# Optimization experiments

Measured on AMD Instinct MI355X. Metric: run time of the kernel, lower is better.

Reference implementation:

```python
import jax, jax.numpy as jnp
import numpy as np

B, T, S, G, D, H, W, CHUNK = 2, 4096, 4096, 64, 1024, 16, 512, 256
HD = D // H


def setup_inputs() -> dict:
    key = jax.random.key(0)
    ks = jax.random.split(key, 16)
    std = 1.0 / np.sqrt(D)
    w = lambda k: jax.random.normal(k, (D, D), jnp.float32) * std
    b = lambda k: jax.random.normal(k, (D,), jnp.float32) * 0.01
    return {
        "query": jax.random.normal(ks[0], (B, T, D), jnp.float32),
        "encoder_out": jax.random.normal(ks[1], (B, S, D), jnp.float32),
        "global_tokens": jax.random.normal(ks[2], (B, G, D), jnp.float32),
        "qw": w(ks[3]), "qb": b(ks[4]),
        "kw": w(ks[5]), "kb": b(ks[6]),
        "vw": w(ks[7]), "vb": b(ks[8]),
        "gkw": w(ks[9]), "gkb": b(ks[10]),
        "gvw": w(ks[11]), "gvb": b(ks[12]),
        "ow": w(ks[13]), "ob": b(ks[14]),
        "compression_ratio": 1,
    }


def reference(query, encoder_out, global_tokens, qw, qb, kw, kb, vw, vb,
              gkw, gkb, gvw, gvb, ow, ob, compression_ratio):
    scale = jnp.float32(np.sqrt(HD))
    r = jnp.float32(compression_ratio)
    # expected raw position for each decoder step, clamped to valid src range
    expected = jnp.clip((jnp.arange(T, dtype=jnp.float32) / r).astype(jnp.int32), 0, S - 1)
    expected = jnp.broadcast_to(expected[None], (B, T))  # [B,T]

    lin = lambda x, wt, bs: x @ wt.T + bs  # torch nn.Linear: y = x W^T + b
    q = lin(query, qw, qb).reshape(B, T, H, HD).transpose(0, 2, 1, 3)            # [B,H,T,HD]
    gk = lin(global_tokens, gkw, gkb).reshape(B, G, H, HD).transpose(0, 2, 1, 3)  # [B,H,G,HD]
    gv = lin(global_tokens, gvw, gvb).reshape(B, G, H, HD).transpose(0, 2, 1, 3)
    ak = lin(encoder_out, kw, kb).reshape(B, S, H, HD).transpose(0, 2, 1, 3)      # [B,H,S,HD]
    av = lin(encoder_out, vw, vb).reshape(B, S, H, HD).transpose(0, 2, 1, 3)

    nC = T // CHUNK
    # per-(batch,chunk) window start, from the middle query's expected position
    centers = expected.reshape(B, nC, CHUNK)[:, :, CHUNK // 2]   # [B,nC]
    win_start = jnp.clip(centers - W // 2, 0, S - W)             # [B,nC]; window always full length W
    idx = win_start[:, :, None] + jnp.arange(W)[None, None, :]   # [B,nC,W]

    gather = lambda kv_b, idx_b: kv_b[:, idx_b, :]               # [H,S,HD],[nC,W] -> [H,nC,W,HD]
    wk = jax.vmap(gather)(ak, idx)                               # [B,H,nC,W,HD]
    wv = jax.vmap(gather)(av, idx)

    qc = q.reshape(B, H, nC, CHUNK, HD)
    sg = jnp.einsum('bhcqd,bhgd->bhcqg', qc, gk) / scale          # global scores  [B,H,nC,CHUNK,G]
    sl = jnp.einsum('bhcqd,bhcwd->bhcqw', qc, wk) / scale         # windowed scores [B,H,nC,CHUNK,W]
    attn = jax.nn.softmax(jnp.concatenate([sg, sl], axis=-1), axis=-1)
    out = (jnp.einsum('bhcqg,bhgd->bhcqd', attn[..., :G], gv)
           + jnp.einsum('bhcqw,bhcwd->bhcqd', attn[..., G:], wv))  # [B,H,nC,CHUNK,HD]
    out = out.reshape(B, H, T, HD).transpose(0, 2, 1, 3).reshape(B, T, D)
    return lin(out, ow, ob)
```

## Files before the change

kernel.cpp:

```cpp
#include <hip/hip_runtime.h>

typedef unsigned short u16;
typedef unsigned int u32;
typedef __attribute__((ext_vector_type(4))) float f32x4;
typedef __attribute__((ext_vector_type(16))) float f32x16;
typedef __attribute__((ext_vector_type(8))) short bf16x8;

constexpr int B_ = 2, T_ = 4096, S_ = 4096, G_ = 64, D_ = 1024, H_ = 16, W_ = 512, CHUNK_ = 256;
constexpr int NC_ = T_ / CHUNK_;
constexpr int NT_ = (G_ + W_) / 32;

__device__ __forceinline__ u16 f2bf(float x) {
  u32 u = __builtin_bit_cast(u32, x);
  return (u16)((u + 0x7FFFu + ((u >> 16) & 1u)) >> 16);
}

__global__ __launch_bounds__(256) void cvt_all_kernel(const float* __restrict__ q, const float* __restrict__ e,
                                                      const float* __restrict__ g, const float* __restrict__ w0,
                                                      const float* __restrict__ w1, const float* __restrict__ w2,
                                                      const float* __restrict__ w3, const float* __restrict__ w4,
                                                      const float* __restrict__ w5, u16* __restrict__ dst) {
  int blk = blockIdx.x;
  const float* src;
  int sblk;
  if (blk < 8192) { src = q; sblk = 0; }
  else if (blk < 16384) { src = e; sblk = 8192; }
  else if (blk < 16512) { src = g; sblk = 16384; }
  else if (blk < 17536) { src = w0; sblk = 16512; }
  else if (blk < 18560) { src = w1; sblk = 17536; }
  else if (blk < 19584) { src = w2; sblk = 18560; }
  else if (blk < 20608) { src = w3; sblk = 19584; }
  else if (blk < 21632) { src = w4; sblk = 20608; }
  else { src = w5; sblk = 21632; }
  int li = (blk - sblk) * 256 + threadIdx.x;
  size_t gi = (size_t)blk * 256 + threadIdx.x;
  float4 v = ((const float4*)src)[li];
  uint2 o;
  o.x = (u32)f2bf(v.x) | ((u32)f2bf(v.y) << 16);
  o.y = (u32)f2bf(v.z) | ((u32)f2bf(v.w) << 16);
  ((uint2*)dst)[gi] = o;
}

__global__ __launch_bounds__(512, 2) void proj_kernel(const u16* __restrict__ ex, const u16* __restrict__ qx,
                                                      const u16* __restrict__ gx, const u16* __restrict__ wgt,
                                                      const float* __restrict__ qb, const float* __restrict__ kbias,
                                                      const float* __restrict__ vbias, const float* __restrict__ gkb,
                                                      const float* __restrict__ gvb, u16* __restrict__ q_bf,
                                                      u16* __restrict__ k_bf, u16* __restrict__ gk_bf) {
  __shared__ char lds[73728];
  constexpr size_t NW = (size_t)D_ * D_;
  constexpr size_t NQs = (size_t)B_ * T_ * D_;
  constexpr size_t NGs = (size_t)B_ * G_ * D_;
  const int tid = threadIdx.x;
  const int lane = tid & 63;
  const int wid = tid >> 6;
  const int wm = wid >> 1, wn = wid & 1;
  const int l15 = lane & 15, kg = lane >> 4;

  const int bid = blockIdx.x;
  const u16 *A, *Bt;
  const float *b1, *b2;
  u16* out;
  int row0, col0, mloc;
  bool scale = false, dual = false;
  size_t dsplit = 0;
  if (bid < 512) {
    row0 = (bid & 31) * 256; col0 = (bid >> 5) * 128; mloc = 256;
    A = ex; Bt = wgt + NW; b1 = kbias; b2 = vbias; out = k_bf; dsplit = NQs; dual = true;
  } else if (bid < 768) {
    int i = bid - 512;
    row0 = (i & 31) * 256; col0 = (i >> 5) * 128; mloc = 256;
    A = qx; Bt = wgt; b1 = qb; b2 = qb; out = q_bf; scale = true;
  } else {
    int i = bid - 768;
    row0 = 0; col0 = i * 128; mloc = 128;
    A = gx; Bt = wgt + 3 * NW; b1 = gkb; b2 = gvb; out = gk_bf; dsplit = NGs; dual = true;
  }
  const float* bp = b1;
  u16* op = out;
  if (dual && col0 >= 1024) { bp = b2 - 1024; op = out + (dsplit - 1024); }

  f32x4 acc[4][4];
#pragma unroll
  for (int i = 0; i < 4; i++)
#pragma unroll
    for (int j = 0; j < 4; j++)
#pragma unroll
      for (int r = 0; r < 4; r++) acc[i][j][r] = 0.f;

  const char* Abase = (const char*)A;
  const char* Bbase = (const char*)Bt;
  const int swb = 16 * ((tid & 3) ^ ((tid >> 3) & 3));

  auto stageA = [&](int slot, int kt) {
#pragma unroll
    for (int p = 0; p < 2; p++) {
      int dst = slot * 16384 + p * 8192 + tid * 16;
      const char* g = Abase + (size_t)(row0 + p * 128 + (tid >> 2)) * 2048 + kt * 64 + swb;
      __builtin_amdgcn_global_load_lds((const __attribute__((address_space(1))) void*)g,
                                       (__attribute__((address_space(3))) void*)(lds + dst), 16, 0, 0);
    }
  };
  auto stageB = [&](int slot, int kt) {
    int dst = 49152 + slot * 8192 + tid * 16;
    const char* g = Bbase + (size_t)(col0 + (tid >> 2)) * 2048 + kt * 64 + swb;
    __builtin_amdgcn_global_load_lds((const __attribute__((address_space(1))) void*)g,
                                     (__attribute__((address_space(3))) void*)(lds + dst), 16, 0, 0);
  };

  stageA(0, 0); stageB(0, 0);
  stageA(1, 1); stageB(1, 1);
  asm volatile("s_waitcnt vmcnt(3)" ::: "memory");
  __builtin_amdgcn_s_barrier();

  int cur = 0, nx = 2;
  for (int t = 0; t < 32; ++t) {
    const char* Ab = lds + cur * 16384;
    const char* Bb = lds + 49152 + cur * 8192;
    if (t + 2 < 32) { stageA(nx, t + 2); stageB(nx, t + 2); }
    bf16x8 bq[4], af[4];
#pragma unroll
    for (int ni = 0; ni < 4; ni++) {
      int r = wn * 64 + ni * 16 + l15;
      bq[ni] = *(const bf16x8*)(Bb + ((r * 64 + kg * 16) ^ (((r >> 1) & 3) << 4)));
    }
#pragma unroll
    for (int mi = 0; mi < 4; mi++) {
      int r = wm * 64 + mi * 16 + l15;
      af[mi] = *(const bf16x8*)(Ab + ((r * 64 + kg * 16) ^ (((r >> 1) & 3) << 4)));
    }
    __builtin_amdgcn_s_setprio(1);
#pragma unroll
    for (int mi = 0; mi < 4; mi++)
#pragma unroll
      for (int ni = 0; ni < 4; ni++)
        acc[mi][ni] = __builtin_amdgcn_mfma_f32_16x16x32_bf16(bq[ni], af[mi], acc[mi][ni], 0, 0, 0);
    __builtin_amdgcn_s_setprio(0);
    if (t < 30) {
      asm volatile("s_waitcnt vmcnt(3)" ::: "memory");
    } else if (t == 30) {
      asm volatile("s_waitcnt vmcnt(0)" ::: "memory");
    }
    __builtin_amdgcn_s_barrier();
    cur = cur == 2 ? 0 : cur + 1;
    nx = nx == 2 ? 0 : nx + 1;
  }

  float4 bv4[4];
#pragma unroll
  for (int ni = 0; ni < 4; ni++) bv4[ni] = *(const float4*)&bp[col0 + wn * 64 + ni * 16 + kg * 4];
#pragma unroll
  for (int mi = 0; mi < 4; mi++) {
    int rloc = wm * 64 + mi * 16 + l15;
    if (rloc >= mloc) continue;
    size_t grow = (size_t)(row0 + rloc);
#pragma unroll
    for (int ni = 0; ni < 4; ni++) {
      int gcol = col0 + wn * 64 + ni * 16 + kg * 4;
      float v0 = acc[mi][ni][0] + bv4[ni].x;
      float v1 = acc[mi][ni][1] + bv4[ni].y;
      float v2 = acc[mi][ni][2] + bv4[ni].z;
      float v3 = acc[mi][ni][3] + bv4[ni].w;
      if (scale) {
        v0 *= 0.18033688011112042f; v1 *= 0.18033688011112042f;
        v2 *= 0.18033688011112042f; v3 *= 0.18033688011112042f;
      }
      uint2 o;
      asm("v_cvt_pk_bf16_f32 %0, %1, %2" : "=v"(o.x) : "v"(v0), "v"(v1));
      asm("v_cvt_pk_bf16_f32 %0, %1, %2" : "=v"(o.y) : "v"(v2), "v"(v3));
      *(uint2*)&op[grow * 1024 + gcol] = o;
    }
  }
}

__global__ __launch_bounds__(512, 2) void gemmO_kernel(const u16* __restrict__ A, const u16* __restrict__ Bt,
                                                       const float* __restrict__ bias, float* __restrict__ out) {
  __shared__ char lds[73728];
  const int tid = threadIdx.x;
  const int lane = tid & 63;
  const int wid = tid >> 6;
  const int wm = wid >> 1, wn = wid & 1;
  const int l15 = lane & 15, kg = lane >> 4;

  const int bid = blockIdx.x;
  const int row0 = (bid & 31) * 256;
  const int col0 = (bid >> 5) * 128;

  f32x4 acc[4][4];
#pragma unroll
  for (int i = 0; i < 4; i++)
#pragma unroll
    for (int j = 0; j < 4; j++)
#pragma unroll
      for (int r = 0; r < 4; r++) acc[i][j][r] = 0.f;

  const char* Abase = (const char*)A;
  const char* Bbase = (const char*)Bt;
  const int swb = 16 * ((tid & 3) ^ ((tid >> 3) & 3));

  auto stageA = [&](int slot, int kt) {
#pragma unroll
    for (int p = 0; p < 2; p++) {
      int dst = slot * 16384 + p * 8192 + tid * 16;
      const char* g = Abase + (size_t)(row0 + p * 128 + (tid >> 2)) * 2048 + kt * 64 + swb;
      __builtin_amdgcn_global_load_lds((const __attribute__((address_space(1))) void*)g,
                                       (__attribute__((address_space(3))) void*)(lds + dst), 16, 0, 0);
    }
  };
  auto stageB = [&](int slot, int kt) {
    int dst = 49152 + slot * 8192 + tid * 16;
    const char* g = Bbase + (size_t)(col0 + (tid >> 2)) * 2048 + kt * 64 + swb;
    __builtin_amdgcn_global_load_lds((const __attribute__((address_space(1))) void*)g,
                                     (__attribute__((address_space(3))) void*)(lds + dst), 16, 0, 0);
  };

  stageA(0, 0); stageB(0, 0);
  stageA(1, 1); stageB(1, 1);
  asm volatile("s_waitcnt vmcnt(3)" ::: "memory");
  __builtin_amdgcn_s_barrier();

  int cur = 0, nx = 2;
  for (int t = 0; t < 32; ++t) {
    const char* Ab = lds + cur * 16384;
    const char* Bb = lds + 49152 + cur * 8192;
    if (t + 2 < 32) { stageA(nx, t + 2); stageB(nx, t + 2); }
    bf16x8 bq[4], af[4];
#pragma unroll
    for (int ni = 0; ni < 4; ni++) {
      int r = wn * 64 + ni * 16 + l15;
      bq[ni] = *(const bf16x8*)(Bb + ((r * 64 + kg * 16) ^ (((r >> 1) & 3) << 4)));
    }
#pragma unroll
    for (int mi = 0; mi < 4; mi++) {
      int r = wm * 64 + mi * 16 + l15;
      af[mi] = *(const bf16x8*)(Ab + ((r * 64 + kg * 16) ^ (((r >> 1) & 3) << 4)));
    }
    __builtin_amdgcn_s_setprio(1);
#pragma unroll
    for (int mi = 0; mi < 4; mi++)
#pragma unroll
      for (int ni = 0; ni < 4; ni++)
        acc[mi][ni] = __builtin_amdgcn_mfma_f32_16x16x32_bf16(bq[ni], af[mi], acc[mi][ni], 0, 0, 0);
    __builtin_amdgcn_s_setprio(0);
    if (t < 30) {
      asm volatile("s_waitcnt vmcnt(3)" ::: "memory");
    } else if (t == 30) {
      asm volatile("s_waitcnt vmcnt(0)" ::: "memory");
    }
    __builtin_amdgcn_s_barrier();
    cur = cur == 2 ? 0 : cur + 1;
    nx = nx == 2 ? 0 : nx + 1;
  }

  float4 bv4[4];
#pragma unroll
  for (int ni = 0; ni < 4; ni++) bv4[ni] = *(const float4*)&bias[col0 + wn * 64 + ni * 16 + kg * 4];
#pragma unroll
  for (int mi = 0; mi < 4; mi++) {
    size_t grow = (size_t)(row0 + wm * 64 + mi * 16 + l15);
#pragma unroll
    for (int ni = 0; ni < 4; ni++) {
      int gcol = col0 + wn * 64 + ni * 16 + kg * 4;
      float4 fo;
      fo.x = acc[mi][ni][0] + bv4[ni].x;
      fo.y = acc[mi][ni][1] + bv4[ni].y;
      fo.z = acc[mi][ni][2] + bv4[ni].z;
      fo.w = acc[mi][ni][3] + bv4[ni].w;
      *(float4*)&out[grow * 1024 + gcol] = fo;
    }
  }
}

__global__ __launch_bounds__(512, 4) void attn_kernel(const u16* __restrict__ q_bf, const u16* __restrict__ k_bf,
                                                      const u16* __restrict__ v_bf, const u16* __restrict__ gk_bf,
                                                      const u16* __restrict__ gv_bf, u16* __restrict__ ao,
                                                      const int* __restrict__ rptr) {
  __shared__ u16 smem[16384];
  const int c = blockIdx.x, h = blockIdx.y, b = blockIdx.z;
  const int tid = threadIdx.x;
  const int lane = tid & 63, wv = tid >> 6;
  const int l31 = lane & 31, half = lane >> 5;
  const int t0 = c * CHUNK_;

  int rr = rptr[0];
  int centert = c * CHUNK_ + CHUNK_ / 2;
  int expected = (int)((float)centert / (float)rr);
  expected = min(max(expected, 0), S_ - 1);
  int ws0 = min(max(expected - W_ / 2, 0), S_ - W_);

  bf16x8 qf[4];
  {
    const u16* qrow = q_bf + ((size_t)(b * T_ + t0 + wv * 32 + l31)) * D_ + h * 64 + half * 8;
#pragma unroll
    for (int s = 0; s < 4; s++) qf[s] = *(const bf16x8*)(qrow + s * 16);
  }

  const int skey = (tid & 255) >> 3, shq = tid & 7;
  const bool isK = tid < 256;

  auto load_tile = [&](int j) -> uint4 {
    const u16* base;
    size_t row;
    if (j < 2) {
      base = isK ? gk_bf : gv_bf;
      row = (size_t)(b * G_ + j * 32 + skey);
    } else {
      base = isK ? k_bf : v_bf;
      row = (size_t)(b * S_ + ws0 + (j - 2) * 32 + skey);
    }
    return *(const uint4*)(base + row * D_ + h * 64 + shq * 8);
  };

  f32x16 oacc[2];
#pragma unroll
  for (int i = 0; i < 2; i++)
#pragma unroll
    for (int r = 0; r < 16; r++) oacc[i][r] = 0.f;
  float mrun = -1e30f, lsum = 0.f;

  uint4 stg = load_tile(0);

  for (int j = 0; j < NT_; j++) {
    const int bsel = j & 1;
    if (isK) {
      *(uint4*)((char*)smem + bsel * 4096 + ((skey * 128 + shq * 16) ^ ((skey & 7) << 4))) = stg;
    } else {
      const u16* pv = (const u16*)&stg;
      char* bp = (char*)smem + 8192 + bsel * 5248 + shq * 656 + skey * 2;
#pragma unroll
      for (int e = 0; e < 8; e++) *(u16*)(bp + e * 80) = pv[e];
    }
    if (j + 1 < NT_) stg = load_tile(j + 1);
    __syncthreads();

    const int kbase = bsel * 4096;
    const int vtb = 8192 + bsel * 5248;

    f32x16 sacc;
#pragma unroll
    for (int r = 0; r < 16; r++) sacc[r] = 0.f;
    __builtin_amdgcn_s_setprio(1);
#pragma unroll
    for (int s = 0; s < 4; s++) {
      int kbx = kbase + ((l31 * 128 + half * 16 + s * 32) ^ ((l31 & 7) << 4));
      bf16x8 kf = *(const bf16x8*)((char*)smem + kbx);
      sacc = __builtin_amdgcn_mfma_f32_32x32x16_bf16(kf, qf[s], sacc, 0, 0, 0);
    }
    __builtin_amdgcn_s_setprio(0);

    float t0m = fmaxf(fmaxf(sacc[0], sacc[1]), sacc[2]);
    float t1m = fmaxf(fmaxf(sacc[3], sacc[4]), sacc[5]);
    float t2m = fmaxf(fmaxf(sacc[6], sacc[7]), sacc[8]);
    float t3m = fmaxf(fmaxf(sacc[9], sacc[10]), sacc[11]);
    float t4m = fmaxf(fmaxf(sacc[12], sacc[13]), sacc[14]);
    float tmax = fmaxf(fmaxf(fmaxf(t0m, t1m), fmaxf(t2m, t3m)), fmaxf(t4m, sacc[15]));
    tmax = fmaxf(tmax, __shfl_xor(tmax, 32));
    if (__any(tmax > mrun + 8.f)) {
      float mnew = fmaxf(mrun, tmax);
      float fac = __builtin_amdgcn_exp2f(mrun - mnew);
      mrun = mnew;
      lsum *= fac;
#pragma unroll
      for (int i = 0; i < 2; i++)
#pragma unroll
        for (int r = 0; r < 16; r++) oacc[i][r] *= fac;
    }
    float p[16];
#pragma unroll
    for (int r = 0; r < 16; r++) p[r] = __builtin_amdgcn_exp2f(sacc[r] - mrun);
    float s0s = (p[0] + p[1]) + (p[2] + p[3]);
    float s1s = (p[4] + p[5]) + (p[6] + p[7]);
    float s2s = (p[8] + p[9]) + (p[10] + p[11]);
    float s3s = (p[12] + p[13]) + (p[14] + p[15]);
    float tsum = (s0s + s1s) + (s2s + s3s);
    tsum += __shfl_xor(tsum, 32);
    lsum += tsum;

    u32 xs[8], px[8];
#pragma unroll
    for (int i = 0; i < 8; i++)
      asm("v_cvt_pk_bf16_f32 %0, %1, %2" : "=v"(xs[i]) : "v"(p[2 * i]), "v"(p[2 * i + 1]));
#pragma unroll
    for (int i = 0; i < 8; i++) px[i] = (u32)__shfl_xor((int)xs[i], 32);
    u32 Bk[2][4];
    Bk[0][0] = half ? px[2] : xs[0];
    Bk[0][1] = half ? px[3] : xs[1];
    Bk[0][2] = half ? xs[2] : px[0];
    Bk[0][3] = half ? xs[3] : px[1];
    Bk[1][0] = half ? px[6] : xs[4];
    Bk[1][1] = half ? px[7] : xs[5];
    Bk[1][2] = half ? xs[6] : px[4];
    Bk[1][3] = half ? xs[7] : px[5];

    int vro = vtb + l31 * 80 + ((l31 >> 3) << 4) + half * 16;
    __builtin_amdgcn_s_setprio(1);
#pragma unroll
    for (int hdf = 0; hdf < 2; hdf++) {
#pragma unroll
      for (int ks = 0; ks < 2; ks++) {
        bf16x8 vf = *(const bf16x8*)((const char*)smem + vro + hdf * 2624 + ks * 32);
        uint4 u4;
        u4.x = Bk[ks][0]; u4.y = Bk[ks][1]; u4.z = Bk[ks][2]; u4.w = Bk[ks][3];
        bf16x8 pb = __builtin_bit_cast(bf16x8, u4);
        oacc[hdf] = __builtin_amdgcn_mfma_f32_32x32x16_bf16(vf, pb, oacc[hdf], 0, 0, 0);
      }
    }
    __builtin_amdgcn_s_setprio(0);
  }

  __syncthreads();
  float inv = 1.f / lsum;
#pragma unroll
  for (int hdf = 0; hdf < 2; hdf++) {
#pragma unroll
    for (int a = 0; a < 4; a++) {
      float f0 = oacc[hdf][4 * a] * inv, f1 = oacc[hdf][4 * a + 1] * inv;
      float f2 = oacc[hdf][4 * a + 2] * inv, f3 = oacc[hdf][4 * a + 3] * inv;
      uint2 o;
      asm("v_cvt_pk_bf16_f32 %0, %1, %2" : "=v"(o.x) : "v"(f0), "v"(f1));
      asm("v_cvt_pk_bf16_f32 %0, %1, %2" : "=v"(o.y) : "v"(f2), "v"(f3));
      int off = wv * 4096 + l31 * 128 + ((16 * a + 8 * half + 64 * hdf) ^ ((l31 & 7) << 4));
      *(uint2*)((char*)smem + off) = o;
    }
  }
  __syncthreads();
#pragma unroll
  for (int it = 0; it < 4; it++) {
    int byteo = (tid + it * 512) * 16;
    int row = byteo >> 7;
    int colb = byteo & 127;
    uint4 vv = *(const uint4*)((const char*)smem + row * 128 + (colb ^ ((row & 7) << 4)));
    *(uint4*)(ao + ((size_t)(b * T_ + t0 + row)) * D_ + h * 64 + (colb >> 1)) = vv;
  }
}

extern "C" void kernel_launch(void* const* d_in, const int* in_sizes, int n_in,
                              void* d_out, int out_size, void* d_ws, size_t ws_size,
                              hipStream_t stream) {
  (void)in_sizes; (void)n_in; (void)out_size; (void)ws_size;
  const float* query = (const float*)d_in[0];
  const float* enc = (const float*)d_in[1];
  const float* glob = (const float*)d_in[2];
  const float* qw = (const float*)d_in[3];
  const float* qb = (const float*)d_in[4];
  const float* kw = (const float*)d_in[5];
  const float* kb = (const float*)d_in[6];
  const float* vw = (const float*)d_in[7];
  const float* vb = (const float*)d_in[8];
  const float* gkw = (const float*)d_in[9];
  const float* gkb = (const float*)d_in[10];
  const float* gvw = (const float*)d_in[11];
  const float* gvb = (const float*)d_in[12];
  const float* ow = (const float*)d_in[13];
  const float* ob = (const float*)d_in[14];
  const int* rp = (const int*)d_in[15];

  const size_t NQ = (size_t)B_ * T_ * D_;
  const size_t NG = (size_t)B_ * G_ * D_;
  const size_t NW = (size_t)D_ * D_;

  u16* ws = (u16*)d_ws;
  u16* qx = ws;
  u16* ex = qx + NQ;
  u16* gx = ex + NQ;
  u16* wgt = gx + NG;
  u16* q_bf = wgt + 6 * NW;
  u16* k_bf = q_bf + NQ;
  u16* v_bf = k_bf + NQ;
  u16* gk_bf = v_bf + NQ;
  u16* gv_bf = gk_bf + NG;
  u16* ao = gv_bf + NG;

  cvt_all_kernel<<<22656, 256, 0, stream>>>(query, enc, glob, qw, kw, vw, gkw, gvw, ow, ws);

  proj_kernel<<<784, 512, 0, stream>>>(ex, qx, gx, wgt, qb, kb, vb, gkb, gvb, q_bf, k_bf, gk_bf);

  attn_kernel<<<dim3(NC_, H_, B_), 512, 0, stream>>>(q_bf, k_bf, v_bf, gk_bf, gv_bf, ao, rp);

  gemmO_kernel<<<256, 512, 0, stream>>>(ao, wgt + 5 * NW, ob, (float*)d_out);
}
```

Baseline: 151.2 us.

## Fuse fp32-to-bf16 activation conversion into projection GEMM A-tile loading

After: 300.8 us. 98.9% more time.

```diff
diff --git a/kernel.cpp b/kernel.cpp
--- a/kernel.cpp
+++ b/kernel.cpp
@@ -15,34 +15,22 @@
   return (u16)((u + 0x7FFFu + ((u >> 16) & 1u)) >> 16);
 }
 
-__global__ __launch_bounds__(256) void cvt_all_kernel(const float* __restrict__ q, const float* __restrict__ e,
-                                                      const float* __restrict__ g, const float* __restrict__ w0,
-                                                      const float* __restrict__ w1, const float* __restrict__ w2,
-                                                      const float* __restrict__ w3, const float* __restrict__ w4,
-                                                      const float* __restrict__ w5, u16* __restrict__ dst) {
+__global__ __launch_bounds__(256) void cvt_w_kernel(const float* w0, const float* w1, const float* w2,
+                                                    const float* w3, const float* w4, const float* w5,
+                                                    u16* __restrict__ dst) {
+  const float* ss[6] = {w0, w1, w2, w3, w4, w5};
   int blk = blockIdx.x;
-  const float* src;
-  int sblk;
-  if (blk < 8192) { src = q; sblk = 0; }
-  else if (blk < 16384) { src = e; sblk = 8192; }
-  else if (blk < 16512) { src = g; sblk = 16384; }
-  else if (blk < 17536) { src = w0; sblk = 16512; }
-  else if (blk < 18560) { src = w1; sblk = 17536; }
-  else if (blk < 19584) { src = w2; sblk = 18560; }
-  else if (blk < 20608) { src = w3; sblk = 19584; }
-  else if (blk < 21632) { src = w4; sblk = 20608; }
-  else { src = w5; sblk = 21632; }
-  int li = (blk - sblk) * 256 + threadIdx.x;
-  size_t gi = (size_t)blk * 256 + threadIdx.x;
-  float4 v = ((const float4*)src)[li];
+  const float4* sp = (const float4*)ss[blk >> 10];
+  int li = (blk & 1023) * 256 + threadIdx.x;
+  float4 v = sp[li];
   uint2 o;
   o.x = (u32)f2bf(v.x) | ((u32)f2bf(v.y) << 16);
   o.y = (u32)f2bf(v.z) | ((u32)f2bf(v.w) << 16);
-  ((uint2*)dst)[gi] = o;
-}
-
-__global__ __launch_bounds__(512, 2) void proj_kernel(const u16* __restrict__ ex, const u16* __restrict__ qx,
-                                                      const u16* __restrict__ gx, const u16* __restrict__ wgt,
+  ((uint2*)dst)[(size_t)blk * 256 + threadIdx.x] = o;
+}
+
+__global__ __launch_bounds__(512, 4) void proj_kernel(const float* __restrict__ enc_f, const float* __restrict__ query_f,
+                                                      const float* __restrict__ glob_f, const u16* __restrict__ wgt,
                                                       const float* __restrict__ qb, const float* __restrict__ kbias,
                                                       const float* __restrict__ vbias, const float* __restrict__ gkb,
                                                       const float* __restrict__ gvb, u16* __restrict__ q_bf,
@@ -58,23 +46,24 @@
   const int l15 = lane & 15, kg = lane >> 4;
 
   const int bid = blockIdx.x;
-  const u16 *A, *Bt;
+  const float* Af;
+  const u16* Bt;
   const float *b1, *b2;
   u16* out;
-  int row0, col0, mloc;
+  int row0, col0, mloc, arowmax;
   bool scale = false, dual = false;
   size_t dsplit = 0;
   if (bid < 512) {
-    row0 = (bid & 31) * 256; col0 = (bid >> 5) * 128; mloc = 256;
-    A = ex; Bt = wgt + NW; b1 = kbias; b2 = vbias; out = k_bf; dsplit = NQs; dual = true;
+    row0 = (bid & 31) * 256; col0 = (bid >> 5) * 128; mloc = 256; arowmax = 8191;
+    Af = enc_f; Bt = wgt + NW; b1 = kbias; b2 = vbias; out = k_bf; dsplit = NQs; dual = true;
   } else if (bid < 768) {
     int i = bid - 512;
-    row0 = (i & 31) * 256; col0 = (i >> 5) * 128; mloc = 256;
-    A = qx; Bt = wgt; b1 = qb; b2 = qb; out = q_bf; scale = true;
+    row0 = (i & 31) * 256; col0 = (i >> 5) * 128; mloc = 256; arowmax = 8191;
+    Af = query_f; Bt = wgt; b1 = qb; b2 = qb; out = q_bf; scale = true;
   } else {
     int i = bid - 768;
-    row0 = 0; col0 = i * 128; mloc = 128;
-    A = gx; Bt = wgt + 3 * NW; b1 = gkb; b2 = gvb; out = gk_bf; dsplit = NGs; dual = true;
+    row0 = 0; col0 = i * 128; mloc = 128; arowmax = 127;
+    Af = glob_f; Bt = wgt + 3 * NW; b1 = gkb; b2 = gvb; out = gk_bf; dsplit = NGs; dual = true;
   }
   const float* bp = b1;
   u16* op = out;
@@ -88,17 +77,33 @@
 #pragma unroll
       for (int r = 0; r < 4; r++) acc[i][j][r] = 0.f;
 
-  const char* Abase = (const char*)A;
+  const char* Ab8 = (const char*)Af;
   const char* Bbase = (const char*)Bt;
   const int swb = 16 * ((tid & 3) ^ ((tid >> 3) & 3));
 
-  auto stageA = [&](int slot, int kt) {
+  auto loadA = [&](int kt, uint4* r) {
 #pragma unroll
     for (int p = 0; p < 2; p++) {
-      int dst = slot * 16384 + p * 8192 + tid * 16;
-      const char* g = Abase + (size_t)(row0 + p * 128 + (tid >> 2)) * 2048 + kt * 64 + swb;
-      __builtin_amdgcn_global_load_lds((const __attribute__((address_space(1))) void*)g,
-                                       (__attribute__((address_space(3))) void*)(lds + dst), 16, 0, 0);
+      int gr = row0 + p * 128 + (tid >> 2);
+      gr = min(gr, arowmax);
+      const char* g = Ab8 + (size_t)gr * 4096 + (size_t)kt * 128 + (tid & 3) * 32;
+      r[p * 2] = *(const uint4*)g;
+      r[p * 2 + 1] = *(const uint4*)(g + 16);
+    }
+  };
+  auto writeA = [&](int slot, const uint4* r) {
+#pragma unroll
+    for (int p = 0; p < 2; p++) {
+      float4 fa = __builtin_bit_cast(float4, r[p * 2]);
+      float4 fb = __builtin_bit_cast(float4, r[p * 2 + 1]);
+      u32 o0, o1, o2, o3;
+      asm("v_cvt_pk_bf16_f32 %0, %1, %2" : "=v"(o0) : "v"(fa.x), "v"(fa.y));
+      asm("v_cvt_pk_bf16_f32 %0, %1, %2" : "=v"(o1) : "v"(fa.z), "v"(fa.w));
+      asm("v_cvt_pk_bf16_f32 %0, %1, %2" : "=v"(o2) : "v"(fb.x), "v"(fb.y));
+      asm("v_cvt_pk_bf16_f32 %0, %1, %2" : "=v"(o3) : "v"(fb.z), "v"(fb.w));
+      uint4 w;
+      w.x = o0; w.y = o1; w.z = o2; w.w = o3;
+      *(uint4*)(lds + slot * 16384 + (p * 128 + (tid >> 2)) * 64 + swb) = w;
     }
   };
   auto stageB = [&](int slot, int kt) {
@@ -108,16 +113,25 @@
                                      (__attribute__((address_space(3))) void*)(lds + dst), 16, 0, 0);
   };
 
-  stageA(0, 0); stageB(0, 0);
-  stageA(1, 1); stageB(1, 1);
-  asm volatile("s_waitcnt vmcnt(3)" ::: "memory");
+  uint4 rX[4], rY[4];
+  loadA(0, rY); stageB(0, 0);
+  loadA(1, rX); stageB(1, 1);
+  asm volatile("s_waitcnt vmcnt(5)" ::: "memory");
+  writeA(0, rY);
+  asm volatile("s_waitcnt lgkmcnt(0)" ::: "memory");
   __builtin_amdgcn_s_barrier();
 
-  int cur = 0, nx = 2;
-  for (int t = 0; t < 32; ++t) {
-    const char* Ab = lds + cur * 16384;
-    const char* Bb = lds + 49152 + cur * 8192;
-    if (t + 2 < 32) { stageA(nx, t + 2); stageB(nx, t + 2); }
+  auto tile = [&](int t, uint4* rcur, uint4* rnext) {
+    if (t + 2 < 32) { loadA(t + 2, rnext); stageB((t + 2) % 3, t + 2); }
+    if (t < 30) {
+      asm volatile("s_waitcnt vmcnt(5)" ::: "memory");
+    } else if (t == 30) {
+      asm volatile("s_waitcnt vmcnt(0)" ::: "memory");
+    }
+    if (t + 1 < 32) writeA((t + 1) % 3, rcur);
+
+    const char* Ab = lds + (t % 3) * 16384;
+    const char* Bb = lds + 49152 + (t % 3) * 8192;
     bf16x8 bq[4], af[4];
 #pragma unroll
     for (int ni = 0; ni < 4; ni++) {
@@ -136,14 +150,13 @@
       for (int ni = 0; ni < 4; ni++)
         acc[mi][ni] = __builtin_amdgcn_mfma_f32_16x16x32_bf16(bq[ni], af[mi], acc[mi][ni], 0, 0, 0);
     __builtin_amdgcn_s_setprio(0);
-    if (t < 30) {
-      asm volatile("s_waitcnt vmcnt(3)" ::: "memory");
-    } else if (t == 30) {
-      asm volatile("s_waitcnt vmcnt(0)" ::: "memory");
-    }
+    asm volatile("s_waitcnt lgkmcnt(0)" ::: "memory");
     __builtin_amdgcn_s_barrier();
-    cur = cur == 2 ? 0 : cur + 1;
-    nx = nx == 2 ? 0 : nx + 1;
+  };
+
+  for (int tt = 0; tt < 32; tt += 2) {
+    tile(tt, rX, rY);
+    tile(tt + 1, rY, rX);
   }
 
   float4 bv4[4];
@@ -460,10 +473,7 @@
   const size_t NW = (size_t)D_ * D_;
 
   u16* ws = (u16*)d_ws;
-  u16* qx = ws;
-  u16* ex = qx + NQ;
-  u16* gx = ex + NQ;
-  u16* wgt = gx + NG;
+  u16* wgt = ws + 2 * NQ + NG;
   u16* q_bf = wgt + 6 * NW;
   u16* k_bf = q_bf + NQ;
   u16* v_bf = k_bf + NQ;
@@ -471,9 +481,9 @@
   u16* gv_bf = gk_bf + NG;
   u16* ao = gv_bf + NG;
 
-  cvt_all_kernel<<<22656, 256, 0, stream>>>(query, enc, glob, qw, kw, vw, gkw, gvw, ow, ws);
-
-  proj_kernel<<<784, 512, 0, stream>>>(ex, qx, gx, wgt, qb, kb, vb, gkb, gvb, q_bf, k_bf, gk_bf);
+  cvt_w_kernel<<<6144, 256, 0, stream>>>(qw, kw, vw, gkw, gvw, ow, wgt);
+
+  proj_kernel<<<784, 512, 0, stream>>>(enc, query, glob, wgt, qb, kb, vb, gkb, gvb, q_bf, k_bf, gk_bf);
 
   attn_kernel<<<dim3(NC_, H_, B_), 512, 0, stream>>>(q_bf, k_bf, v_bf, gk_bf, gv_bf, ao, rp);
 
```
